# Performance work log

Hardware: AMD Instinct MI355X
Metric: run time of the kernel (lower is better)

## Reference

```python
import jax, jax.numpy as jnp
import numpy as np

B, N, NIN, NHID, D = 8, 2048, 256, 256, 64  # head = 1 (required by squeeze())


def setup_inputs() -> dict:
    key = jax.random.key(0)
    ks = jax.random.split(key, 12)
    xn = lambda k, shape, s=1.0: jax.random.normal(k, shape, jnp.float32) * s
    xav = lambda fi, fo: (2.0 / (fi + fo)) ** 0.5  # xavier_normal std
    return {
        "inputs": xn(ks[0], (B, N, NIN)),
        "fc1_w": xn(ks[1], (NHID, NIN), xav(NIN, NHID)),
        "fc1_b": jnp.full((NHID,), 0.1, jnp.float32),
        "fc2_w": xn(ks[2], (NHID, NHID), xav(NHID, NHID)),
        "fc2_b": jnp.full((NHID,), 0.1, jnp.float32),
        "bn_g": 1.0 + 0.1 * xn(ks[3], (NHID,)),
        "bn_b": 0.1 * xn(ks[4], (NHID,)),
        "bn_mean": 0.1 * xn(ks[5], (NHID,)),
        "bn_var": jax.random.uniform(ks[6], (NHID,), jnp.float32, 0.5, 1.5),
        "wq_w": xn(ks[7], (D, NHID), xav(NHID, D)),
        "wq_b": jnp.full((D,), 0.1, jnp.float32),
        "wk_w": xn(ks[8], (D, NHID), xav(NHID, D)),
        "wk_b": jnp.full((D,), 0.1, jnp.float32),
        "mlp2_w": xn(ks[9], (1, 2 * D), xav(2 * D, 1)),
        "mlp2_b": jnp.full((1,), 0.1, jnp.float32),
    }


def reference(inputs, fc1_w, fc1_b, fc2_w, fc2_b, bn_g, bn_b, bn_mean, bn_var,
              wq_w, wq_b, wk_w, wk_b, mlp2_w, mlp2_b):
    # MLP: Linear -> ELU -> (dropout off, eval) -> Linear -> ELU -> BatchNorm1d (eval, running stats)
    x = jax.nn.elu(jnp.einsum('bni,hi->bnh', inputs, fc1_w) + fc1_b)
    x = jax.nn.elu(jnp.einsum('bnh,oh->bno', x, fc2_w) + fc2_b)
    X = (x - bn_mean) * jax.lax.rsqrt(bn_var + 1e-5) * bn_g + bn_b  # [B,N,NHID]
    # Q/K projections (head=1 -> shapes [B,N,D])
    Xq = jnp.einsum('bnh,dh->bnd', X, wq_w) + wq_b
    Xk = jnp.einsum('bnh,dh->bnd', X, wk_w) + wk_b
    # Original: cat([NK, NQ], -1) over all (i,j) pairs then Linear(2D -> 1).
    # Algebraically identical decomposition: probs[b,i,j] = Xk[b,j].wk_half + Xq[b,i].wq_half + bias
    wk_half, wq_half = mlp2_w[0, :D], mlp2_w[0, D:]
    sk = Xk @ wk_half  # [B,N]  (varies with j, the K/column index)
    sq = Xq @ wq_half  # [B,N]  (varies with i, the Q/row index)
    probs = sq[:, :, None] + sk[:, None, :] + mlp2_b[0]  # [B,N,N]
    return probs
```

## Files before the change

### kernel.cpp

```cpp
#include <hip/hip_runtime.h>
#include <hip/hip_bf16.h>
#include <math.h>

typedef __bf16 bf16x8 __attribute__((ext_vector_type(8)));
typedef float  f32x4  __attribute__((ext_vector_type(4)));
typedef unsigned int u32;
typedef u32 u32x4 __attribute__((ext_vector_type(4)));
typedef unsigned short u16;

#define WS_UQ    0
#define WS_UK    256
#define WS_CONST 512
#define WS_SQ    528
#define WS_SK    16912

__device__ __forceinline__ float elu1(float x) {
    return x > 0.f ? x : (__expf(x) - 1.f);
}

__device__ __forceinline__ void gload16(const void* g, void* l) {
    __builtin_amdgcn_global_load_lds((const __attribute__((address_space(1))) void*)g,
                                     (__attribute__((address_space(3))) void*)l,
                                     16, 0, 0);
}

__global__ void prep_all(const float* __restrict__ w1, const float* __restrict__ w2,
                         const float* __restrict__ bn_g, const float* __restrict__ bn_b,
                         const float* __restrict__ bn_mean, const float* __restrict__ bn_var,
                         const float* __restrict__ wq_w, const float* __restrict__ wq_b,
                         const float* __restrict__ wk_w, const float* __restrict__ wk_b,
                         const float* __restrict__ mlp2_w, const float* __restrict__ mlp2_b,
                         float* __restrict__ ws, float* __restrict__ outb) {
    if (blockIdx.x == 0) {
        __shared__ float redq[256], redk[256];
        const int h = threadIdx.x;
        float s  = bn_g[h] * rsqrtf(bn_var[h] + 1e-5f);
        float tt = bn_b[h] - bn_mean[h] * s;
        float vq = 0.f, vk = 0.f;
        #pragma unroll
        for (int d = 0; d < 64; ++d) {
            vq += wq_w[d * 256 + h] * mlp2_w[64 + d];
            vk += wk_w[d * 256 + h] * mlp2_w[d];
        }
        ws[WS_UQ + h] = s * vq;
        ws[WS_UK + h] = s * vk;
        redq[h] = tt * vq;
        redk[h] = tt * vk;
        __syncthreads();
        for (int st = 128; st > 0; st >>= 1) {
            if (h < st) { redq[h] += redq[h + st]; redk[h] += redk[h + st]; }
            __syncthreads();
        }
        if (h == 0) {
            float cq = 0.f, ck = 0.f;
            for (int d = 0; d < 64; ++d) {
                cq += wq_b[d] * mlp2_w[64 + d];
                ck += wk_b[d] * mlp2_w[d];
            }
            ws[WS_CONST + 0] = redq[0] + cq;
            ws[WS_CONST + 1] = redk[0] + ck;
            ws[WS_CONST + 2] = mlp2_b[0];
        }
        return;
    }
    const int bid = blockIdx.x - 1;
    const int m   = bid >> 3;
    const int kt  = bid & 7;
    const float* src = m ? w2 : w1;
    __bf16* stg = (__bf16*)outb + m * 65536;
    const int tid = threadIdx.x;
    #pragma unroll
    for (int it = 0; it < 4; ++it) {
        int idx = it * 256 + tid;
        int nt = idx >> 6, l = idx & 63;
        int lr = l & 15, lk = l >> 4;
        const float* sp = src + (nt * 16 + lr) * 256 + kt * 32 + lk * 8;
        bf16x8 hi;
        #pragma unroll
        for (int j = 0; j < 8; ++j) hi[j] = (__bf16)sp[j];
        *(bf16x8*)(stg + (kt * 16 + nt) * 512 + l * 8) = hi;
    }
}

__global__ __launch_bounds__(256) void main_mfma(const float* __restrict__ inp,
                                                 const float* __restrict__ b1,
                                                 const float* __restrict__ b2,
                                                 float* __restrict__ ws,
                                                 const float* __restrict__ outb) {
    __shared__ u32 LDSu[8192];
    __shared__ float redq[128], redk[128];

    const int tid = threadIdx.x;
    const int l   = tid & 63;
    const int w   = tid >> 6;
    const int lr  = l & 15;
    const int lk  = l >> 4;
    const int rows0 = blockIdx.x * 32;
    const int n0  = w * 64;

    const __bf16* s1 = (const __bf16*)outb;
    const __bf16* s2 = s1 + 65536;

    {
        const char* inb = (const char*)(inp + (size_t)rows0 * 256);
        #pragma unroll
        for (int j = 0; j < 8; ++j) {
            int row = w * 8 + j;
            int srcb = row * 1024 + ((l * 16) ^ ((row & 15) << 4));
            gload16(inb + srcb, ((char*)LDSu) + row * 1024 + l * 16);
        }
    }

    f32x4 acc[2][4];
    #pragma unroll
    for (int p = 0; p < 2; ++p)
        #pragma unroll
        for (int nt = 0; nt < 4; ++nt) acc[p][nt] = (f32x4)0.f;

    bf16x8 bc[4];
    #pragma unroll
    for (int nt = 0; nt < 4; ++nt)
        bc[nt] = *(const bf16x8*)(s1 + ((0 * 16 + w * 4 + nt) << 9) + l * 8);

    __syncthreads();

    const int sw = lr << 4;

    #pragma unroll
    for (int kt = 0; kt < 8; ++kt) {
        bf16x8 bn[4];
        if (kt < 7) {
            #pragma unroll
            for (int nt = 0; nt < 4; ++nt)
                bn[nt] = *(const bf16x8*)(s1 + (((kt + 1) * 16 + w * 4 + nt) << 9) + l * 8);
        } else {
            #pragma unroll
            for (int nt = 0; nt < 4; ++nt) bn[nt] = bc[nt];
        }
        int cb = kt * 128 + lk * 32;
        bf16x8 ah[2], al[2];
        #pragma unroll
        for (int p = 0; p < 2; ++p) {
            int base = (p * 16 + lr) * 1024;
            float4 f0 = *(const float4*)((const char*)LDSu + base + (cb ^ sw));
            float4 f1 = *(const float4*)((const char*)LDSu + base + ((cb + 16) ^ sw));
            float fv[8] = {f0.x,f0.y,f0.z,f0.w,f1.x,f1.y,f1.z,f1.w};
            #pragma unroll
            for (int j = 0; j < 8; ++j) {
                __bf16 hv = (__bf16)fv[j];
                ah[p][j] = hv;
                al[p][j] = (__bf16)(fv[j] - (float)hv);
            }
        }
        #pragma unroll
        for (int p = 0; p < 2; ++p)
            #pragma unroll
            for (int nt = 0; nt < 4; ++nt) {
                acc[p][nt] = __builtin_amdgcn_mfma_f32_16x16x32_bf16(ah[p], bc[nt], acc[p][nt], 0, 0, 0);
                acc[p][nt] = __builtin_amdgcn_mfma_f32_16x16x32_bf16(al[p], bc[nt], acc[p][nt], 0, 0, 0);
            }
        #pragma unroll
        for (int nt = 0; nt < 4; ++nt) bc[nt] = bn[nt];
    }

    __syncthreads();

    #pragma unroll
    for (int p = 0; p < 2; ++p)
        #pragma unroll
        for (int nt = 0; nt < 4; ++nt) {
            int col = n0 + nt * 16 + lr;
            float bb = b1[col];
            #pragma unroll
            for (int r = 0; r < 4; ++r) {
                int row = p * 16 + lk * 4 + r;
                float v = elu1(acc[p][nt][r] + bb);
                __bf16 hv = (__bf16)v;
                __bf16 lv = (__bf16)(v - (float)hv);
                u32 pk = ((u32)__builtin_bit_cast(u16, hv) << 16) | __builtin_bit_cast(u16, lv);
                int ob = row * 1024 + ((col * 4) ^ ((row & 15) << 4));
                *(u32*)((char*)LDSu + ob) = pk;
            }
        }
    __syncthreads();

    #pragma unroll
    for (int p = 0; p < 2; ++p)
        #pragma unroll
        for (int nt = 0; nt < 4; ++nt) acc[p][nt] = (f32x4)0.f;

    bf16x8 bc2[4];
    #pragma unroll
    for (int nt = 0; nt < 4; ++nt)
        bc2[nt] = *(const bf16x8*)(s2 + ((0 * 16 + w * 4 + nt) << 9) + l * 8);

    #pragma unroll
    for (int kt = 0; kt < 8; ++kt) {
        bf16x8 bn[4];
        if (kt < 7) {
            #pragma unroll
            for (int nt = 0; nt < 4; ++nt)
                bn[nt] = *(const bf16x8*)(s2 + (((kt + 1) * 16 + w * 4 + nt) << 9) + l * 8);
        } else {
            #pragma unroll
            for (int nt = 0; nt < 4; ++nt) bn[nt] = bc2[nt];
        }
        int cb = kt * 128 + lk * 32;
        bf16x8 ah[2], al[2];
        #pragma unroll
        for (int p = 0; p < 2; ++p) {
            int base = (p * 16 + lr) * 1024;
            u32x4 q0 = *(const u32x4*)((const char*)LDSu + base + (cb ^ sw));
            u32x4 q1 = *(const u32x4*)((const char*)LDSu + base + ((cb + 16) ^ sw));
            u32 hw0 = __builtin_amdgcn_perm(q0.y, q0.x, 0x07060302u);
            u32 hw1 = __builtin_amdgcn_perm(q0.w, q0.z, 0x07060302u);
            u32 hw2 = __builtin_amdgcn_perm(q1.y, q1.x, 0x07060302u);
            u32 hw3 = __builtin_amdgcn_perm(q1.w, q1.z, 0x07060302u);
            u32 lw0 = __builtin_amdgcn_perm(q0.y, q0.x, 0x05040100u);
            u32 lw1 = __builtin_amdgcn_perm(q0.w, q0.z, 0x05040100u);
            u32 lw2 = __builtin_amdgcn_perm(q1.y, q1.x, 0x05040100u);
            u32 lw3 = __builtin_amdgcn_perm(q1.w, q1.z, 0x05040100u);
            u32x4 hh = {hw0, hw1, hw2, hw3};
            u32x4 ll = {lw0, lw1, lw2, lw3};
            ah[p] = __builtin_bit_cast(bf16x8, hh);
            al[p] = __builtin_bit_cast(bf16x8, ll);
        }
        #pragma unroll
        for (int p = 0; p < 2; ++p)
            #pragma unroll
            for (int nt = 0; nt < 4; ++nt) {
                acc[p][nt] = __builtin_amdgcn_mfma_f32_16x16x32_bf16(ah[p], bc2[nt], acc[p][nt], 0, 0, 0);
                acc[p][nt] = __builtin_amdgcn_mfma_f32_16x16x32_bf16(al[p], bc2[nt], acc[p][nt], 0, 0, 0);
            }
        #pragma unroll
        for (int nt = 0; nt < 4; ++nt) bc2[nt] = bn[nt];
    }

    float sqp[2][4] = {{0.f,0.f,0.f,0.f},{0.f,0.f,0.f,0.f}};
    float skp[2][4] = {{0.f,0.f,0.f,0.f},{0.f,0.f,0.f,0.f}};
    const float* uq = ws + WS_UQ;
    const float* uk = ws + WS_UK;
    #pragma unroll
    for (int p = 0; p < 2; ++p)
        #pragma unroll
        for (int nt = 0; nt < 4; ++nt) {
            int col = n0 + nt * 16 + lr;
            float bb = b2[col], qc = uq[col], kc = uk[col];
            #pragma unroll
            for (int r = 0; r < 4; ++r) {
                float v = elu1(acc[p][nt][r] + bb);
                sqp[p][r] += v * qc;
                skp[p][r] += v * kc;
            }
        }
    #pragma unroll
    for (int mm = 8; mm >= 1; mm >>= 1) {
        #pragma unroll
        for (int p = 0; p < 2; ++p)
            #pragma unroll
            for (int r = 0; r < 4; ++r) {
                sqp[p][r] += __shfl_xor(sqp[p][r], mm);
                skp[p][r] += __shfl_xor(skp[p][r], mm);
            }
    }
    if (lr == 0) {
        #pragma unroll
        for (int p = 0; p < 2; ++p)
            #pragma unroll
            for (int r = 0; r < 4; ++r) {
                int row = p * 16 + lk * 4 + r;
                redq[w * 32 + row] = sqp[p][r];
                redk[w * 32 + row] = skp[p][r];
            }
    }
    __syncthreads();
    if (tid < 32) {
        float s = ws[WS_CONST + 0];
        #pragma unroll
        for (int ww = 0; ww < 4; ++ww) s += redq[ww * 32 + tid];
        ws[WS_SQ + rows0 + tid] = s;
    } else if (tid < 64) {
        int rl = tid - 32;
        float s = ws[WS_CONST + 1];
        #pragma unroll
        for (int ww = 0; ww < 4; ++ww) s += redk[ww * 32 + rl];
        ws[WS_SK + rows0 + rl] = s;
    }
}

__global__ __launch_bounds__(256) void broadcast_out(const float* __restrict__ ws,
                                                     float* __restrict__ out) {
    __shared__ float skL[2048];
    const int bi = blockIdx.x;
    const int b = bi >> 8;
    const int chunk = bi & 255;
    const int tid = threadIdx.x;

    float4* skL4 = (float4*)skL;
    const float4* skb4 = (const float4*)(ws + WS_SK + b * 2048);
    #pragma unroll
    for (int it = 0; it < 2; ++it) skL4[it * 256 + tid] = skb4[it * 256 + tid];
    __syncthreads();

    const float mb = ws[WS_CONST + 2];
    const int i0 = chunk * 8;
    #pragma unroll
    for (int i = 0; i < 8; ++i) {
        float sval = ws[WS_SQ + b * 2048 + i0 + i] + mb;
        float4* orow = (float4*)(out + ((size_t)(b * 2048 + i0 + i)) * 2048);
        #pragma unroll
        for (int hh = 0; hh < 2; ++hh) {
            int j4 = hh * 256 + tid;
            float4 v = skL4[j4];
            orow[j4] = make_float4(sval + v.x, sval + v.y, sval + v.z, sval + v.w);
        }
    }
}

extern "C" void kernel_launch(void* const* d_in, const int* in_sizes, int n_in,
                              void* d_out, int out_size, void* d_ws, size_t ws_size,
                              hipStream_t stream) {
    const float* inputs  = (const float*)d_in[0];
    const float* fc1_w   = (const float*)d_in[1];
    const float* fc1_b   = (const float*)d_in[2];
    const float* fc2_w   = (const float*)d_in[3];
    const float* fc2_b   = (const float*)d_in[4];
    const float* bn_g    = (const float*)d_in[5];
    const float* bn_b    = (const float*)d_in[6];
    const float* bn_mean = (const float*)d_in[7];
    const float* bn_var  = (const float*)d_in[8];
    const float* wq_w    = (const float*)d_in[9];
    const float* wq_b    = (const float*)d_in[10];
    const float* wk_w    = (const float*)d_in[11];
    const float* wk_b    = (const float*)d_in[12];
    const float* mlp2_w  = (const float*)d_in[13];
    const float* mlp2_b  = (const float*)d_in[14];
    float* ws  = (float*)d_ws;
    float* out = (float*)d_out;

    hipLaunchKernelGGL(prep_all, dim3(17), dim3(256), 0, stream,
                       fc1_w, fc2_w, bn_g, bn_b, bn_mean, bn_var,
                       wq_w, wq_b, wk_w, wk_b, mlp2_w, mlp2_b, ws, out);
    hipLaunchKernelGGL(main_mfma, dim3(512), dim3(256), 0, stream,
                       inputs, fc1_b, fc2_b, ws, out);
    hipLaunchKernelGGL(broadcast_out, dim3(2048), dim3(256), 0, stream, ws, out);
}
```

Before: 47.22 us.

## Fuse weight prep into main MFMA kernel, converting fp32 weights in-register

Removes the separate prep kernel that pre-converted fc1/fc2 weights to bf16 and computed the BN/Q/K folding constants. Each block of the main kernel now recomputes the folded vectors itself and reads fp32 weights directly from global memory, converting them to bf16 in registers with a one-step prefetch. This drops one kernel launch and its serialization, but every one of 512 blocks redoes the 64-term dot products and reads twice the weight bytes.

```diff
diff --git a/kernel.cpp b/kernel.cpp
--- a/kernel.cpp
+++ b/kernel.cpp
@@ -8,11 +8,8 @@
 typedef u32 u32x4 __attribute__((ext_vector_type(4)));
 typedef unsigned short u16;
 
-#define WS_UQ    0
-#define WS_UK    256
-#define WS_CONST 512
-#define WS_SQ    528
-#define WS_SK    16912
+#define WS_SQ    0
+#define WS_SK    16384
 
 __device__ __forceinline__ float elu1(float x) {
     return x > 0.f ? x : (__expf(x) - 1.f);
@@ -24,71 +21,27 @@
                                      16, 0, 0);
 }
 
-__global__ void prep_all(const float* __restrict__ w1, const float* __restrict__ w2,
-                         const float* __restrict__ bn_g, const float* __restrict__ bn_b,
-                         const float* __restrict__ bn_mean, const float* __restrict__ bn_var,
-                         const float* __restrict__ wq_w, const float* __restrict__ wq_b,
-                         const float* __restrict__ wk_w, const float* __restrict__ wk_b,
-                         const float* __restrict__ mlp2_w, const float* __restrict__ mlp2_b,
-                         float* __restrict__ ws, float* __restrict__ outb) {
-    if (blockIdx.x == 0) {
-        __shared__ float redq[256], redk[256];
-        const int h = threadIdx.x;
-        float s  = bn_g[h] * rsqrtf(bn_var[h] + 1e-5f);
-        float tt = bn_b[h] - bn_mean[h] * s;
-        float vq = 0.f, vk = 0.f;
-        #pragma unroll
-        for (int d = 0; d < 64; ++d) {
-            vq += wq_w[d * 256 + h] * mlp2_w[64 + d];
-            vk += wk_w[d * 256 + h] * mlp2_w[d];
-        }
-        ws[WS_UQ + h] = s * vq;
-        ws[WS_UK + h] = s * vk;
-        redq[h] = tt * vq;
-        redk[h] = tt * vk;
-        __syncthreads();
-        for (int st = 128; st > 0; st >>= 1) {
-            if (h < st) { redq[h] += redq[h + st]; redk[h] += redk[h + st]; }
-            __syncthreads();
-        }
-        if (h == 0) {
-            float cq = 0.f, ck = 0.f;
-            for (int d = 0; d < 64; ++d) {
-                cq += wq_b[d] * mlp2_w[64 + d];
-                ck += wk_b[d] * mlp2_w[d];
-            }
-            ws[WS_CONST + 0] = redq[0] + cq;
-            ws[WS_CONST + 1] = redk[0] + ck;
-            ws[WS_CONST + 2] = mlp2_b[0];
-        }
-        return;
-    }
-    const int bid = blockIdx.x - 1;
-    const int m   = bid >> 3;
-    const int kt  = bid & 7;
-    const float* src = m ? w2 : w1;
-    __bf16* stg = (__bf16*)outb + m * 65536;
-    const int tid = threadIdx.x;
-    #pragma unroll
-    for (int it = 0; it < 4; ++it) {
-        int idx = it * 256 + tid;
-        int nt = idx >> 6, l = idx & 63;
-        int lr = l & 15, lk = l >> 4;
-        const float* sp = src + (nt * 16 + lr) * 256 + kt * 32 + lk * 8;
-        bf16x8 hi;
-        #pragma unroll
-        for (int j = 0; j < 8; ++j) hi[j] = (__bf16)sp[j];
-        *(bf16x8*)(stg + (kt * 16 + nt) * 512 + l * 8) = hi;
-    }
-}
-
-__global__ __launch_bounds__(256) void main_mfma(const float* __restrict__ inp,
-                                                 const float* __restrict__ b1,
-                                                 const float* __restrict__ b2,
-                                                 float* __restrict__ ws,
-                                                 const float* __restrict__ outb) {
+__device__ __forceinline__ bf16x8 cvt8(float4 f0, float4 f1) {
+    bf16x8 r;
+    r[0] = (__bf16)f0.x; r[1] = (__bf16)f0.y; r[2] = (__bf16)f0.z; r[3] = (__bf16)f0.w;
+    r[4] = (__bf16)f1.x; r[5] = (__bf16)f1.y; r[6] = (__bf16)f1.z; r[7] = (__bf16)f1.w;
+    return r;
+}
+
+__global__ __launch_bounds__(256) void main_fused(
+        const float* __restrict__ inp,
+        const float* __restrict__ w1, const float* __restrict__ w2,
+        const float* __restrict__ b1, const float* __restrict__ b2,
+        const float* __restrict__ bn_g, const float* __restrict__ bn_b,
+        const float* __restrict__ bn_mean, const float* __restrict__ bn_var,
+        const float* __restrict__ wq_w, const float* __restrict__ wq_b,
+        const float* __restrict__ wk_w, const float* __restrict__ wk_b,
+        const float* __restrict__ mlp2_w,
+        float* __restrict__ ws) {
     __shared__ u32 LDSu[8192];
+    __shared__ float uqs[256], uks[256];
     __shared__ float redq[128], redk[128];
+    __shared__ float sred[8];
 
     const int tid = threadIdx.x;
     const int l   = tid & 63;
@@ -97,9 +50,7 @@
     const int lk  = l >> 4;
     const int rows0 = blockIdx.x * 32;
     const int n0  = w * 64;
-
-    const __bf16* s1 = (const __bf16*)outb;
-    const __bf16* s2 = s1 + 65536;
+    const int sw  = lr << 4;
 
     {
         const char* inb = (const char*)(inp + (size_t)rows0 * 256);
@@ -111,31 +62,55 @@
         }
     }
 
+    {
+        const int col = tid;
+        float s  = bn_g[col] * rsqrtf(bn_var[col] + 1e-5f);
+        float tt = bn_b[col] - bn_mean[col] * s;
+        float vq = 0.f, vk = 0.f;
+        #pragma unroll
+        for (int d = 0; d < 64; ++d) {
+            vq += wq_w[d * 256 + col] * mlp2_w[64 + d];
+            vk += wk_w[d * 256 + col] * mlp2_w[d];
+        }
+        uqs[col] = s * vq;
+        uks[col] = s * vk;
+        float rq = tt * vq, rk = tt * vk;
+        #pragma unroll
+        for (int m = 32; m >= 1; m >>= 1) {
+            rq += __shfl_xor(rq, m);
+            rk += __shfl_xor(rk, m);
+        }
+        if (l == 0) { sred[w] = rq; sred[4 + w] = rk; }
+    }
+
+    float4 wr[8];
+    #pragma unroll
+    for (int nt = 0; nt < 4; ++nt) {
+        const float* wp = w1 + (size_t)(n0 + nt * 16 + lr) * 256 + lk * 8;
+        wr[2 * nt]     = ((const float4*)wp)[0];
+        wr[2 * nt + 1] = ((const float4*)wp)[1];
+    }
+
     f32x4 acc[2][4];
     #pragma unroll
     for (int p = 0; p < 2; ++p)
         #pragma unroll
         for (int nt = 0; nt < 4; ++nt) acc[p][nt] = (f32x4)0.f;
 
-    bf16x8 bc[4];
-    #pragma unroll
-    for (int nt = 0; nt < 4; ++nt)
-        bc[nt] = *(const bf16x8*)(s1 + ((0 * 16 + w * 4 + nt) << 9) + l * 8);
-
-    __syncthreads();
-
-    const int sw = lr << 4;
+    __syncthreads();
 
     #pragma unroll
     for (int kt = 0; kt < 8; ++kt) {
-        bf16x8 bn[4];
+        bf16x8 bc[4];
+        #pragma unroll
+        for (int nt = 0; nt < 4; ++nt) bc[nt] = cvt8(wr[2 * nt], wr[2 * nt + 1]);
         if (kt < 7) {
             #pragma unroll
-            for (int nt = 0; nt < 4; ++nt)
-                bn[nt] = *(const bf16x8*)(s1 + (((kt + 1) * 16 + w * 4 + nt) << 9) + l * 8);
-        } else {
-            #pragma unroll
-            for (int nt = 0; nt < 4; ++nt) bn[nt] = bc[nt];
+            for (int nt = 0; nt < 4; ++nt) {
+                const float* wp = w1 + (size_t)(n0 + nt * 16 + lr) * 256 + (kt + 1) * 32 + lk * 8;
+                wr[2 * nt]     = ((const float4*)wp)[0];
+                wr[2 * nt + 1] = ((const float4*)wp)[1];
+            }
         }
         int cb = kt * 128 + lk * 32;
         bf16x8 ah[2], al[2];
@@ -159,8 +134,6 @@
                 acc[p][nt] = __builtin_amdgcn_mfma_f32_16x16x32_bf16(ah[p], bc[nt], acc[p][nt], 0, 0, 0);
                 acc[p][nt] = __builtin_amdgcn_mfma_f32_16x16x32_bf16(al[p], bc[nt], acc[p][nt], 0, 0, 0);
             }
-        #pragma unroll
-        for (int nt = 0; nt < 4; ++nt) bc[nt] = bn[nt];
     }
 
     __syncthreads();
@@ -182,6 +155,13 @@
                 *(u32*)((char*)LDSu + ob) = pk;
             }
         }
+
+    #pragma unroll
+    for (int nt = 0; nt < 4; ++nt) {
+        const float* wp = w2 + (size_t)(n0 + nt * 16 + lr) * 256 + lk * 8;
+        wr[2 * nt]     = ((const float4*)wp)[0];
+        wr[2 * nt + 1] = ((const float4*)wp)[1];
+    }
     __syncthreads();
 
     #pragma unroll
@@ -189,21 +169,18 @@
         #pragma unroll
         for (int nt = 0; nt < 4; ++nt) acc[p][nt] = (f32x4)0.f;
 
-    bf16x8 bc2[4];
-    #pragma unroll
-    for (int nt = 0; nt < 4; ++nt)
-        bc2[nt] = *(const bf16x8*)(s2 + ((0 * 16 + w * 4 + nt) << 9) + l * 8);
-
     #pragma unroll
     for (int kt = 0; kt < 8; ++kt) {
-        bf16x8 bn[4];
+        bf16x8 bc[4];
+        #pragma unroll
+        for (int nt = 0; nt < 4; ++nt) bc[nt] = cvt8(wr[2 * nt], wr[2 * nt + 1]);
         if (kt < 7) {
             #pragma unroll
-            for (int nt = 0; nt < 4; ++nt)
-                bn[nt] = *(const bf16x8*)(s2 + (((kt + 1) * 16 + w * 4 + nt) << 9) + l * 8);
-        } else {
-            #pragma unroll
-            for (int nt = 0; nt < 4; ++nt) bn[nt] = bc2[nt];
+            for (int nt = 0; nt < 4; ++nt) {
+                const float* wp = w2 + (size_t)(n0 + nt * 16 + lr) * 256 + (kt + 1) * 32 + lk * 8;
+                wr[2 * nt]     = ((const float4*)wp)[0];
+                wr[2 * nt + 1] = ((const float4*)wp)[1];
+            }
         }
         int cb = kt * 128 + lk * 32;
         bf16x8 ah[2], al[2];
@@ -229,23 +206,19 @@
         for (int p = 0; p < 2; ++p)
             #pragma unroll
             for (int nt = 0; nt < 4; ++nt) {
-                acc[p][nt] = __builtin_amdgcn_mfma_f32_16x16x32_bf16(ah[p], bc2[nt], acc[p][nt], 0, 0, 0);
-                acc[p][nt] = __builtin_amdgcn_mfma_f32_16x16x32_bf16(al[p], bc2[nt], acc[p][nt], 0, 0, 0);
-            }
-        #pragma unroll
-        for (int nt = 0; nt < 4; ++nt) bc2[nt] = bn[nt];
+                acc[p][nt] = __builtin_amdgcn_mfma_f32_16x16x32_bf16(ah[p], bc[nt], acc[p][nt], 0, 0, 0);
+                acc[p][nt] = __builtin_amdgcn_mfma_f32_16x16x32_bf16(al[p], bc[nt], acc[p][nt], 0, 0, 0);
+            }
     }
 
     float sqp[2][4] = {{0.f,0.f,0.f,0.f},{0.f,0.f,0.f,0.f}};
     float skp[2][4] = {{0.f,0.f,0.f,0.f},{0.f,0.f,0.f,0.f}};
-    const float* uq = ws + WS_UQ;
-    const float* uk = ws + WS_UK;
     #pragma unroll
     for (int p = 0; p < 2; ++p)
         #pragma unroll
         for (int nt = 0; nt < 4; ++nt) {
             int col = n0 + nt * 16 + lr;
-            float bb = b2[col], qc = uq[col], kc = uk[col];
+            float bb = b2[col], qc = uqs[col], kc = uks[col];
             #pragma unroll
             for (int r = 0; r < 4; ++r) {
                 float v = elu1(acc[p][nt][r] + bb);
@@ -275,13 +248,19 @@
     }
     __syncthreads();
     if (tid < 32) {
-        float s = ws[WS_CONST + 0];
+        float dq = sred[0] + sred[1] + sred[2] + sred[3];
+        #pragma unroll
+        for (int d = 0; d < 64; ++d) dq += wq_b[d] * mlp2_w[64 + d];
+        float s = dq;
         #pragma unroll
         for (int ww = 0; ww < 4; ++ww) s += redq[ww * 32 + tid];
         ws[WS_SQ + rows0 + tid] = s;
     } else if (tid < 64) {
         int rl = tid - 32;
-        float s = ws[WS_CONST + 1];
+        float dk = sred[4] + sred[5] + sred[6] + sred[7];
+        #pragma unroll
+        for (int d = 0; d < 64; ++d) dk += wk_b[d] * mlp2_w[d];
+        float s = dk;
         #pragma unroll
         for (int ww = 0; ww < 4; ++ww) s += redk[ww * 32 + rl];
         ws[WS_SK + rows0 + rl] = s;
@@ -289,6 +268,7 @@
 }
 
 __global__ __launch_bounds__(256) void broadcast_out(const float* __restrict__ ws,
+                                                     const float* __restrict__ mlp2_b,
                                                      float* __restrict__ out) {
     __shared__ float skL[2048];
     const int bi = blockIdx.x;
@@ -302,7 +282,7 @@
     for (int it = 0; it < 2; ++it) skL4[it * 256 + tid] = skb4[it * 256 + tid];
     __syncthreads();
 
-    const float mb = ws[WS_CONST + 2];
+    const float mb = mlp2_b[0];
     const int i0 = chunk * 8;
     #pragma unroll
     for (int i = 0; i < 8; ++i) {
@@ -338,10 +318,10 @@
     float* ws  = (float*)d_ws;
     float* out = (float*)d_out;
 
-    hipLaunchKernelGGL(prep_all, dim3(17), dim3(256), 0, stream,
-                       fc1_w, fc2_w, bn_g, bn_b, bn_mean, bn_var,
-                       wq_w, wq_b, wk_w, wk_b, mlp2_w, mlp2_b, ws, out);
-    hipLaunchKernelGGL(main_mfma, dim3(512), dim3(256), 0, stream,
-                       inputs, fc1_b, fc2_b, ws, out);
-    hipLaunchKernelGGL(broadcast_out, dim3(2048), dim3(256), 0, stream, ws, out);
-}
+    hipLaunchKernelGGL(main_fused, dim3(512), dim3(256), 0, stream,
+                       inputs, fc1_w, fc2_w, fc1_b, fc2_b,
+                       bn_g, bn_b, bn_mean, bn_var,
+                       wq_w, wq_b, wk_w, wk_b, mlp2_w, ws);
+    hipLaunchKernelGGL(broadcast_out, dim3(2048), dim3(256), 0, stream,
+                       ws, mlp2_b, out);
+}
```

After: 64.46 us. 1.37x slower.
